# Kernel tuning notes

Measured on AMD Instinct MI355X. Metric: run time of the kernel, lower is better.

## Reference

```python
import jax, jax.numpy as jnp
import numpy as np

HIDDEN = 768
INTER = 2048
N_EXPERTS = 8
TOP_K = 2
SWIGLU_LIMIT = 7.0
N_TOK = 8192


def setup_inputs() -> dict:
    key = jax.random.key(0)
    k_x, k_r, k_gu, k_d = jax.random.split(key, 4)
    x = jax.random.normal(k_x, (N_TOK, HIDDEN), dtype=jnp.float32)
    router_w = jax.random.normal(k_r, (N_EXPERTS, HIDDEN), dtype=jnp.float32) * 0.02
    gate_up_proj = jax.random.normal(k_gu, (N_EXPERTS, 2 * INTER, HIDDEN), dtype=jnp.float32) * 0.02
    down_proj = jax.random.normal(k_d, (N_EXPERTS, HIDDEN, INTER), dtype=jnp.float32) * 0.02
    return {"x": x, "router_w": router_w, "gate_up_proj": gate_up_proj, "down_proj": down_proj}


def reference(x, router_w, gate_up_proj, down_proj):
    # router: [n_tok, E]
    router_logits = x @ router_w.T
    topk_vals, topk_idx = jax.lax.top_k(router_logits, TOP_K)  # [n_tok, k]
    topk_weights = jax.nn.softmax(topk_vals.astype(jnp.float32), axis=-1).astype(x.dtype)

    out = jnp.zeros_like(x)
    # Loop over the small fixed expert set; each expert is a dense GEMM over all
    # tokens, masked by its per-token routing weight (0 for unrouted tokens) —
    # identical math to the original gather/GEMM/scatter dispatch.
    for e in range(N_EXPERTS):
        # per-token weight for expert e (sums slots; each expert appears at most once per token)
        w_e = jnp.sum(jnp.where(topk_idx == e, topk_weights, 0.0), axis=-1)  # [n_tok]
        gate_up = x @ gate_up_proj[e].T  # [n_tok, 2*I]
        gate, up = jnp.split(gate_up, 2, axis=-1)
        up = jnp.minimum(up, SWIGLU_LIMIT)
        mlp_out = (jax.nn.silu(gate) * up) @ down_proj[e].T  # [n_tok, H]
        out = out + mlp_out * w_e[:, None]
    return out
```

## Files before the change

kernel.cpp:

```cpp
#include <hip/hip_runtime.h>
#include <hip/hip_bf16.h>

typedef unsigned short u16;
typedef unsigned int u32;
typedef short bf16x8 __attribute__((ext_vector_type(8)));
typedef float f32x4 __attribute__((ext_vector_type(4)));

#define NTOK 8192
#define HID 768
#define INTER 2048
#define NEXP 8

#define MFMA16(a, b, c) __builtin_amdgcn_mfma_f32_16x16x32_bf16(a, b, c, 0, 0, 0)
#define S_BARRIER() __builtin_amdgcn_s_barrier()
#define SETPRIO(x) __builtin_amdgcn_s_setprio(x)
#define WAITVM(n) asm volatile("s_waitcnt vmcnt(" #n ")" ::: "memory")

__device__ __forceinline__ u16 f2bf(float f) {
    u32 u = __builtin_bit_cast(u32, f);
    u32 r = (u + 0x7FFFu + ((u >> 16) & 1u)) >> 16;
    return (u16)r;
}

__device__ __forceinline__ void gld16(const void* g, void* l) {
    __builtin_amdgcn_global_load_lds((const __attribute__((address_space(1))) void*)g,
                                     (__attribute__((address_space(3))) void*)l, 16, 0, 0);
}

__global__ __launch_bounds__(256) void zero_kernel(float4* out4, int n4) {
    int i = blockIdx.x * blockDim.x + threadIdx.x;
    float4 z = {0.f, 0.f, 0.f, 0.f};
    int stride = gridDim.x * blockDim.x;
    for (int k = i; k < n4; k += stride) out4[k] = z;
}

__global__ __launch_bounds__(256) void cvt_kernel(const float* __restrict__ src, u16* __restrict__ dst, int n8) {
    int i = blockIdx.x * blockDim.x + threadIdx.x;
    int stride = gridDim.x * blockDim.x;
    for (; i < n8; i += stride) {
        const float4* s = (const float4*)(src + (size_t)i * 8);
        float4 a = s[0], b = s[1];
        u16 r[8] = {f2bf(a.x), f2bf(a.y), f2bf(a.z), f2bf(a.w),
                    f2bf(b.x), f2bf(b.y), f2bf(b.z), f2bf(b.w)};
        *(uint4*)(dst + (size_t)i * 8) = *(const uint4*)r;
    }
}

__global__ __launch_bounds__(256) void router2(const float* __restrict__ x, const float* __restrict__ rw,
                                               u32* __restrict__ route, float* __restrict__ wslot) {
    int wv = threadIdx.x >> 6, ln = threadIdx.x & 63;
    int t = blockIdx.x * 4 + wv;
    if (t >= NTOK) return;
    float xr[12];
#pragma unroll
    for (int j = 0; j < 12; j++) xr[j] = x[(size_t)t * HID + ln + j * 64];
    float lg[NEXP];
#pragma unroll
    for (int e = 0; e < NEXP; e++) {
        float a = 0.f;
#pragma unroll
        for (int j = 0; j < 12; j++) a += xr[j] * rw[e * HID + ln + j * 64];
#pragma unroll
        for (int off = 32; off; off >>= 1) a += __shfl_xor(a, off);
        lg[e] = a;
    }
    int i0 = 0;
    float v0 = lg[0];
#pragma unroll
    for (int e = 1; e < NEXP; e++)
        if (lg[e] > v0) { v0 = lg[e]; i0 = e; }
    int i1 = -1;
    float v1 = -1e30f;
#pragma unroll
    for (int e = 0; e < NEXP; e++) {
        if (e == i0) continue;
        if (lg[e] > v1) { v1 = lg[e]; i1 = e; }
    }
    float w0 = 1.f / (1.f + __expf(v1 - v0));
    float w1 = 1.f - w0;
    if (ln == 0) {
        wslot[0 * NTOK + t] = w0;
        wslot[1 * NTOK + t] = w1;
        route[t] = (u32)i0 | ((u32)i1 << 8);
    }
}

__global__ __launch_bounds__(1024) void scatter_kernel(const u32* __restrict__ route, int* __restrict__ counts,
                                                       int* __restrict__ tokslot, int* __restrict__ ntiles,
                                                       int* __restrict__ tiledesc) {
    __shared__ int sc[NEXP][1024];
    int tid = threadIdx.x;
    u32 rt[8];
    int cnt[NEXP] = {0, 0, 0, 0, 0, 0, 0, 0};
#pragma unroll
    for (int k = 0; k < 8; k++) {
        rt[k] = route[tid * 8 + k];
        cnt[rt[k] & 255]++;
        cnt[(rt[k] >> 8) & 255]++;
    }
#pragma unroll
    for (int e = 0; e < NEXP; e++) sc[e][tid] = cnt[e];
    __syncthreads();
    for (int off = 1; off < 1024; off <<= 1) {
        int v[NEXP];
#pragma unroll
        for (int e = 0; e < NEXP; e++) v[e] = (tid >= off) ? sc[e][tid - off] : 0;
        __syncthreads();
#pragma unroll
        for (int e = 0; e < NEXP; e++)
            if (tid >= off) sc[e][tid] += v[e];
        __syncthreads();
    }
    int base[NEXP];
#pragma unroll
    for (int e = 0; e < NEXP; e++) base[e] = sc[e][tid] - cnt[e];
#pragma unroll
    for (int k = 0; k < 8; k++) {
        int t = tid * 8 + k;
        int e0 = rt[k] & 255, e1 = (rt[k] >> 8) & 255;
        tokslot[e0 * NTOK + base[e0]] = t;
        base[e0]++;
        tokslot[e1 * NTOK + base[e1]] = t | (1 << 16);
        base[e1]++;
    }
    if (tid == 0) {
        int tot = 0;
        for (int e = 0; e < NEXP; e++) {
            int c = sc[e][1023];
            counts[e] = c;
            int nt = (c + 255) >> 8;
            for (int q = 0; q < nt; q++) tiledesc[tot++] = (e << 8) | q;
        }
        ntiles[0] = tot;
    }
}


#define STAGE8(d, kt)                                        \
    do {                                                     \
        char* dA_ = lds + (d)*65536 + tid * 16;              \
        char* dB_ = dA_ + 32768;                             \
        size_t ko_ = (size_t)(kt)*128;                       \
        gld16(aP[0] + ko_, dA_);                             \
        gld16(aP[1] + ko_, dA_ + 8192);                      \
        gld16(aP[2] + ko_, dA_ + 16384);                     \
        gld16(aP[3] + ko_, dA_ + 24576);                     \
        gld16(bP[0] + ko_, dB_);                             \
        gld16(bP[1] + ko_, dB_ + 8192);                      \
        gld16(bP[2] + ko_, dB_ + 16384);                     \
        gld16(bP[3] + ko_, dB_ + 24576);                     \
    } while (0)

#define MMALL()                                                           \
    do {                                                                  \
        _Pragma("unroll") for (int m_ = 0; m_ < 8; m_++)                  \
            _Pragma("unroll") for (int n_ = 0; n_ < 4; n_++)              \
                acc[m_][n_] = MFMA16(af[m_], bfr[n_], acc[m_][n_]);       \
    } while (0)

#define PIPE2(NKT)                                                        \
    f32x4 acc[8][4];                                                      \
    _Pragma("unroll") for (int m_ = 0; m_ < 8; m_++)                      \
        _Pragma("unroll") for (int n_ = 0; n_ < 4; n_++) acc[m_][n_] = (f32x4)0.f; \
    const int aBase = (wr * 128 + rsel) * 128;                            \
    const int bBase = 32768 + (wc * 64 + rsel) * 128;                     \
    const int s0 = ((g4 ^ (rsel & 7)) << 4);                              \
    const int s1 = (((4 + g4) ^ (rsel & 7)) << 4);                        \
    STAGE8(0, 0);                                                         \
    WAITVM(0);                                                            \
    S_BARRIER();                                                          \
    for (int t = 0; t < (NKT); ++t) {                                     \
        if (t + 1 < (NKT)) STAGE8((t + 1) & 1, t + 1);                    \
        const char* Tb = lds + (t & 1) * 65536;                           \
        bf16x8 af[8], bfr[4];                                             \
        _Pragma("unroll") for (int m_ = 0; m_ < 8; m_++)                  \
            af[m_] = *(const bf16x8*)(Tb + aBase + m_ * 2048 + s0);       \
        _Pragma("unroll") for (int n_ = 0; n_ < 4; n_++)                  \
            bfr[n_] = *(const bf16x8*)(Tb + bBase + n_ * 2048 + s0);      \
        SETPRIO(1); MMALL(); SETPRIO(0);                                  \
        _Pragma("unroll") for (int m_ = 0; m_ < 8; m_++)                  \
            af[m_] = *(const bf16x8*)(Tb + aBase + m_ * 2048 + s1);       \
        _Pragma("unroll") for (int n_ = 0; n_ < 4; n_++)                  \
            bfr[n_] = *(const bf16x8*)(Tb + bBase + n_ * 2048 + s1);      \
        SETPRIO(1); MMALL(); SETPRIO(0);                                  \
        WAITVM(0);                                                        \
        S_BARRIER();                                                      \
    }

__global__ __launch_bounds__(512, 2) void gateup2p(const u16* __restrict__ xb, const u16* __restrict__ gub,
                                                   const int* __restrict__ counts,
                                                   const int* __restrict__ ntiles, const int* __restrict__ tiledesc,
                                                   const int* __restrict__ tokslot, u16* __restrict__ h) {
    if ((int)blockIdx.x >= ntiles[0]) return;
    int td = tiledesc[blockIdx.x];
    int e = td >> 8;
    int cnt = counts[e];
    int row0 = (td & 255) * 256;
    int c0 = blockIdx.y * 128;

    extern __shared__ char lds[];
    int tid = threadIdx.x;
    int wv = tid >> 6, ln = tid & 63;
    int wr = wv >> 2, wc = wv & 3;
    int rsel = ln & 15, g4 = ln >> 4;

    int srow = tid >> 3;
    int sswz = ((tid & 7) ^ (srow & 7)) << 4;
    const char* aP[4];
    const char* bP[4];
#pragma unroll
    for (int c = 0; c < 4; c++) {
        int r = c * 64 + srow;
        int gr = row0 + r;
        gr = gr < cnt ? gr : cnt - 1;
        int tok = tokslot[e * NTOK + gr] & 0xFFFF;
        aP[c] = (const char*)xb + (size_t)tok * (HID * 2) + sswz;
        int wi = r & 63;
        int b = (wi >> 5) * 2048 + c0 + (r >> 6) * 32 + (wi & 31);
        bP[c] = (const char*)gub + ((size_t)e * 4096 + b) * (HID * 2) + sswz;
    }

    PIPE2(HID / 64)

#pragma unroll
    for (int mg = 0; mg < 8; mg++) {
#pragma unroll
        for (int j = 0; j < 4; j++) {
            int gr = row0 + wr * 128 + mg * 16 + g4 * 4 + j;
            if (gr >= cnt) continue;
            int ts = tokslot[e * NTOK + gr];
            int tok = ts & 0xFFFF, slot = ts >> 16;
            u16* hrow = h + (size_t)(slot * NTOK + tok) * INTER;
#pragma unroll
            for (int n = 0; n < 2; n++) {
                float gv = acc[mg][n][j];
                float uv = fminf(acc[mg][n + 2][j], 7.0f);
                float sg = gv / (1.0f + __expf(-gv));
                hrow[c0 + wc * 32 + n * 16 + rsel] = f2bf(sg * uv);
            }
        }
    }
}

__global__ __launch_bounds__(512, 2) void down2p(const u16* __restrict__ hb, const u16* __restrict__ dnb,
                                                 const int* __restrict__ counts,
                                                 const int* __restrict__ ntiles, const int* __restrict__ tiledesc,
                                                 const int* __restrict__ tokslot,
                                                 const float* __restrict__ wslot, float* __restrict__ out) {
    if ((int)blockIdx.x >= ntiles[0]) return;
    int td = tiledesc[blockIdx.x];
    int e = td >> 8;
    int cnt = counts[e];
    int row0 = (td & 255) * 256;
    int col0 = blockIdx.y * 256;

    extern __shared__ char lds[];
    int tid = threadIdx.x;
    int wv = tid >> 6, ln = tid & 63;
    int wr = wv >> 2, wc = wv & 3;
    int rsel = ln & 15, g4 = ln >> 4;

    int srow = tid >> 3;
    int sswz = ((tid & 7) ^ (srow & 7)) << 4;
    const char* aP[4];
    const char* bP[4];
#pragma unroll
    for (int c = 0; c < 4; c++) {
        int r = c * 64 + srow;
        int gr = row0 + r;
        gr = gr < cnt ? gr : cnt - 1;
        int ts = tokslot[e * NTOK + gr];
        aP[c] = (const char*)hb + (size_t)((ts >> 16) * NTOK + (ts & 0xFFFF)) * (INTER * 2) + sswz;
        bP[c] = (const char*)dnb + ((size_t)e * HID + col0 + r) * (INTER * 2) + sswz;
    }

    PIPE2(INTER / 64)

#pragma unroll
    for (int mg = 0; mg < 8; mg++) {
#pragma unroll
        for (int j = 0; j < 4; j++) {
            int gr = row0 + wr * 128 + mg * 16 + g4 * 4 + j;
            if (gr >= cnt) continue;
            int ts = tokslot[e * NTOK + gr];
            int tok = ts & 0xFFFF, slot = ts >> 16;
            float w = wslot[slot * NTOK + tok];
#pragma unroll
            for (int n = 0; n < 4; n++) {
                int col = col0 + wc * 64 + n * 16 + rsel;
                atomicAdd(&out[(size_t)tok * HID + col], w * acc[mg][n][j]);
            }
        }
    }
}

extern "C" void kernel_launch(void* const* d_in, const int* in_sizes, int n_in,
                              void* d_out, int out_size, void* d_ws, size_t ws_size,
                              hipStream_t stream) {
    const float* x = (const float*)d_in[0];
    const float* rw = (const float*)d_in[1];
    const float* gu = (const float*)d_in[2];
    const float* dn = (const float*)d_in[3];
    float* out = (float*)d_out;
    char* ws = (char*)d_ws;

    int* counts = (int*)(ws + 0);
    int* ntiles = (int*)(ws + 64);
    int* tiledesc = (int*)(ws + 128);
    int* tokslot = (int*)(ws + 512);
    float* wslot = (float*)(ws + 262656);
    u16* xb = (u16*)(ws + 328192);
    u16* gub = (u16*)(ws + 12911104);
    u16* dnb = (u16*)(ws + 63242752);
    u16* hb = (u16*)(ws + 88408576);
    u32* route = (u32*)(ws + 88408576);

    zero_kernel<<<1024, 256, 0, stream>>>((float4*)out, NTOK * HID / 4);
    cvt_kernel<<<2048, 256, 0, stream>>>(x, xb, NTOK * HID / 8);
    cvt_kernel<<<2048, 256, 0, stream>>>(gu, gub, NEXP * 2 * INTER * HID / 8);
    cvt_kernel<<<2048, 256, 0, stream>>>(dn, dnb, NEXP * HID * INTER / 8);
    router2<<<NTOK / 4, 256, 0, stream>>>(x, rw, route, wslot);
    scatter_kernel<<<1, 1024, 0, stream>>>(route, counts, tokslot, ntiles, tiledesc);
    gateup2p<<<dim3(72, 16), 512, 131072, stream>>>(xb, gub, counts, ntiles, tiledesc, tokslot, hb);
    down2p<<<dim3(72, 3), 512, 131072, stream>>>(hb, dnb, counts, ntiles, tiledesc, tokslot, wslot, out);
}
```

Baseline: 315.4 us.

## Switch GEMM pipeline to 4-stage K=32 LDS ring and swap grid order

```diff
diff --git a/kernel.cpp b/kernel.cpp
--- a/kernel.cpp
+++ b/kernel.cpp
@@ -136,19 +136,15 @@
 }
 
 
-#define STAGE8(d, kt)                                        \
+#define STAGE4(d, kt)                                        \
     do {                                                     \
-        char* dA_ = lds + (d)*65536 + tid * 16;              \
-        char* dB_ = dA_ + 32768;                             \
-        size_t ko_ = (size_t)(kt)*128;                       \
+        char* dA_ = lds + (d)*32768 + tid * 16;              \
+        char* dB_ = dA_ + 16384;                             \
+        size_t ko_ = (size_t)(kt)*64;                        \
         gld16(aP[0] + ko_, dA_);                             \
         gld16(aP[1] + ko_, dA_ + 8192);                      \
-        gld16(aP[2] + ko_, dA_ + 16384);                     \
-        gld16(aP[3] + ko_, dA_ + 24576);                     \
         gld16(bP[0] + ko_, dB_);                             \
         gld16(bP[1] + ko_, dB_ + 8192);                      \
-        gld16(bP[2] + ko_, dB_ + 16384);                     \
-        gld16(bP[3] + ko_, dB_ + 24576);                     \
     } while (0)
 
 #define MMALL()                                                           \
@@ -158,45 +154,42 @@
                 acc[m_][n_] = MFMA16(af[m_], bfr[n_], acc[m_][n_]);       \
     } while (0)
 
-#define PIPE2(NKT)                                                        \
+#define PIPE4(NKT)                                                        \
     f32x4 acc[8][4];                                                      \
     _Pragma("unroll") for (int m_ = 0; m_ < 8; m_++)                      \
         _Pragma("unroll") for (int n_ = 0; n_ < 4; n_++) acc[m_][n_] = (f32x4)0.f; \
-    const int aBase = (wr * 128 + rsel) * 128;                            \
-    const int bBase = 32768 + (wc * 64 + rsel) * 128;                     \
-    const int s0 = ((g4 ^ (rsel & 7)) << 4);                              \
-    const int s1 = (((4 + g4) ^ (rsel & 7)) << 4);                        \
-    STAGE8(0, 0);                                                         \
-    WAITVM(0);                                                            \
+    const int aBase = (wr * 128 + rsel) * 64;                             \
+    const int bBase = 16384 + (wc * 64 + rsel) * 64;                      \
+    const int sOff = ((g4 ^ (rsel & 3) ^ ((rsel >> 2) & 3)) << 4);        \
+    STAGE4(0, 0);                                                         \
+    STAGE4(1, 1);                                                         \
+    STAGE4(2, 2);                                                         \
+    WAITVM(8);                                                            \
     S_BARRIER();                                                          \
     for (int t = 0; t < (NKT); ++t) {                                     \
-        if (t + 1 < (NKT)) STAGE8((t + 1) & 1, t + 1);                    \
-        const char* Tb = lds + (t & 1) * 65536;                           \
+        if (t + 3 < (NKT)) STAGE4((t + 3) & 3, t + 3);                    \
+        const char* Tb = lds + (t & 3) * 32768;                           \
         bf16x8 af[8], bfr[4];                                             \
         _Pragma("unroll") for (int m_ = 0; m_ < 8; m_++)                  \
-            af[m_] = *(const bf16x8*)(Tb + aBase + m_ * 2048 + s0);       \
+            af[m_] = *(const bf16x8*)(Tb + aBase + m_ * 1024 + sOff);     \
         _Pragma("unroll") for (int n_ = 0; n_ < 4; n_++)                  \
-            bfr[n_] = *(const bf16x8*)(Tb + bBase + n_ * 2048 + s0);      \
+            bfr[n_] = *(const bf16x8*)(Tb + bBase + n_ * 1024 + sOff);    \
         SETPRIO(1); MMALL(); SETPRIO(0);                                  \
-        _Pragma("unroll") for (int m_ = 0; m_ < 8; m_++)                  \
-            af[m_] = *(const bf16x8*)(Tb + aBase + m_ * 2048 + s1);       \
-        _Pragma("unroll") for (int n_ = 0; n_ < 4; n_++)                  \
-            bfr[n_] = *(const bf16x8*)(Tb + bBase + n_ * 2048 + s1);      \
-        SETPRIO(1); MMALL(); SETPRIO(0);                                  \
-        WAITVM(0);                                                        \
-        S_BARRIER();                                                      \
-    }
-
-__global__ __launch_bounds__(512, 2) void gateup2p(const u16* __restrict__ xb, const u16* __restrict__ gub,
+        if (t < (NKT)-3) { WAITVM(8); S_BARRIER(); }                      \
+        else if (t == (NKT)-3) { WAITVM(4); S_BARRIER(); }                \
+        else if (t == (NKT)-2) { WAITVM(0); S_BARRIER(); }                \
+    }
+
+__global__ __launch_bounds__(512, 2) void gateup4p(const u16* __restrict__ xb, const u16* __restrict__ gub,
                                                    const int* __restrict__ counts,
                                                    const int* __restrict__ ntiles, const int* __restrict__ tiledesc,
                                                    const int* __restrict__ tokslot, u16* __restrict__ h) {
-    if ((int)blockIdx.x >= ntiles[0]) return;
-    int td = tiledesc[blockIdx.x];
+    if ((int)blockIdx.y >= ntiles[0]) return;
+    int td = tiledesc[blockIdx.y];
     int e = td >> 8;
     int cnt = counts[e];
     int row0 = (td & 255) * 256;
-    int c0 = blockIdx.y * 128;
+    int c0 = blockIdx.x * 128;
 
     extern __shared__ char lds[];
     int tid = threadIdx.x;
@@ -204,13 +197,13 @@
     int wr = wv >> 2, wc = wv & 3;
     int rsel = ln & 15, g4 = ln >> 4;
 
-    int srow = tid >> 3;
-    int sswz = ((tid & 7) ^ (srow & 7)) << 4;
-    const char* aP[4];
-    const char* bP[4];
-#pragma unroll
-    for (int c = 0; c < 4; c++) {
-        int r = c * 64 + srow;
+    int srow = tid >> 2, sl = tid & 3;
+    int sswz = ((sl ^ (srow & 3) ^ ((srow >> 2) & 3)) << 4);
+    const char* aP[2];
+    const char* bP[2];
+#pragma unroll
+    for (int c = 0; c < 2; c++) {
+        int r = c * 128 + srow;
         int gr = row0 + r;
         gr = gr < cnt ? gr : cnt - 1;
         int tok = tokslot[e * NTOK + gr] & 0xFFFF;
@@ -220,7 +213,7 @@
         bP[c] = (const char*)gub + ((size_t)e * 4096 + b) * (HID * 2) + sswz;
     }
 
-    PIPE2(HID / 64)
+    PIPE4(HID / 32)
 
 #pragma unroll
     for (int mg = 0; mg < 8; mg++) {
@@ -242,17 +235,17 @@
     }
 }
 
-__global__ __launch_bounds__(512, 2) void down2p(const u16* __restrict__ hb, const u16* __restrict__ dnb,
+__global__ __launch_bounds__(512, 2) void down4p(const u16* __restrict__ hb, const u16* __restrict__ dnb,
                                                  const int* __restrict__ counts,
                                                  const int* __restrict__ ntiles, const int* __restrict__ tiledesc,
                                                  const int* __restrict__ tokslot,
                                                  const float* __restrict__ wslot, float* __restrict__ out) {
-    if ((int)blockIdx.x >= ntiles[0]) return;
-    int td = tiledesc[blockIdx.x];
+    if ((int)blockIdx.y >= ntiles[0]) return;
+    int td = tiledesc[blockIdx.y];
     int e = td >> 8;
     int cnt = counts[e];
     int row0 = (td & 255) * 256;
-    int col0 = blockIdx.y * 256;
+    int col0 = blockIdx.x * 256;
 
     extern __shared__ char lds[];
     int tid = threadIdx.x;
@@ -260,13 +253,13 @@
     int wr = wv >> 2, wc = wv & 3;
     int rsel = ln & 15, g4 = ln >> 4;
 
-    int srow = tid >> 3;
-    int sswz = ((tid & 7) ^ (srow & 7)) << 4;
-    const char* aP[4];
-    const char* bP[4];
-#pragma unroll
-    for (int c = 0; c < 4; c++) {
-        int r = c * 64 + srow;
+    int srow = tid >> 2, sl = tid & 3;
+    int sswz = ((sl ^ (srow & 3) ^ ((srow >> 2) & 3)) << 4);
+    const char* aP[2];
+    const char* bP[2];
+#pragma unroll
+    for (int c = 0; c < 2; c++) {
+        int r = c * 128 + srow;
         int gr = row0 + r;
         gr = gr < cnt ? gr : cnt - 1;
         int ts = tokslot[e * NTOK + gr];
@@ -274,7 +267,7 @@
         bP[c] = (const char*)dnb + ((size_t)e * HID + col0 + r) * (INTER * 2) + sswz;
     }
 
-    PIPE2(INTER / 64)
+    PIPE4(INTER / 32)
 
 #pragma unroll
     for (int mg = 0; mg < 8; mg++) {
@@ -321,6 +314,6 @@
     cvt_kernel<<<2048, 256, 0, stream>>>(dn, dnb, NEXP * HID * INTER / 8);
     router2<<<NTOK / 4, 256, 0, stream>>>(x, rw, route, wslot);
     scatter_kernel<<<1, 1024, 0, stream>>>(route, counts, tokslot, ntiles, tiledesc);
-    gateup2p<<<dim3(72, 16), 512, 131072, stream>>>(xb, gub, counts, ntiles, tiledesc, tokslot, hb);
-    down2p<<<dim3(72, 3), 512, 131072, stream>>>(hb, dnb, counts, ntiles, tiledesc, tokslot, wslot, out);
-}
+    gateup4p<<<dim3(16, 72), 512, 131072, stream>>>(xb, gub, counts, ntiles, tiledesc, tokslot, hb);
+    down4p<<<dim3(3, 72), 512, 131072, stream>>>(hb, dnb, counts, ntiles, tiledesc, tokslot, wslot, out);
+}
```

Measured after the change: 333.3 us. +5.7%, slower.
